# Optimization experiments

Measured on AMD Instinct MI355X. Metric: run time of the kernel, lower is better.

The kernel has to match this reference:

```python
import jax, jax.numpy as jnp
import numpy as np

N_NODES = 100000
N_EDGES = 3200000
NFEAT = 512
HIDDEN = 256
NCLASS = 64
K = 10
ALPHA = 0.1


def setup_inputs() -> dict:
    key = jax.random.key(0)
    ks = jax.random.split(key, 5)
    x = jax.random.normal(ks[0], (N_NODES, NFEAT), dtype=jnp.float32)
    edge_index = jax.random.randint(ks[1], (2, N_EDGES), 0, N_NODES, dtype=jnp.int64)
    W1 = jax.random.normal(ks[2], (NFEAT, HIDDEN), dtype=jnp.float32) * (1.0 / np.sqrt(NFEAT))
    b1 = jnp.zeros((HIDDEN,), dtype=jnp.float32)
    W2 = jax.random.normal(ks[3], (HIDDEN, NCLASS), dtype=jnp.float32) * (1.0 / np.sqrt(HIDDEN))
    b2 = jnp.zeros((NCLASS,), dtype=jnp.float32)
    # PPR initialization of GPR coefficients: alpha*(1-alpha)^k, last = (1-alpha)^K
    temp_np = ALPHA * (1.0 - ALPHA) ** np.arange(K + 1)
    temp_np[-1] = (1.0 - ALPHA) ** K
    temp = jnp.asarray(temp_np, dtype=jnp.float32)
    return {"x": x, "edge_index": edge_index, "W1": W1, "b1": b1, "W2": W2, "b2": b2, "temp": temp}


def reference(x, edge_index, W1, b1, W2, b2, temp):
    N = x.shape[0]
    # --- gcn_norm: add self-loops, symmetric normalization ---
    loop = jnp.arange(N, dtype=edge_index.dtype)
    row = jnp.concatenate([edge_index[0], loop])  # source nodes
    col = jnp.concatenate([edge_index[1], loop])  # target nodes
    ones = jnp.ones(row.shape[0], dtype=x.dtype)
    deg = jax.ops.segment_sum(ones, col, num_segments=N)
    dinv = jnp.where(deg > 0, jax.lax.rsqrt(deg), jnp.zeros((), x.dtype))
    norm = dinv[row] * dinv[col]  # [E+N]

    # --- MLP (eval mode: dropout is identity) ---
    h = jax.nn.relu(x @ W1 + b1) @ W2 + b2  # [N, nclass]

    # --- GPR propagation: hidden = sum_k temp[k] * (Ahat^k h) ---
    hidden = h * temp[0]
    for k in range(K):
        h = jax.ops.segment_sum(norm[:, None] * h[row], col, num_segments=N)
        hidden = hidden + temp[k + 1] * h

    return jax.nn.log_softmax(hidden, axis=1)
```

## Files before the change

### kernel.cpp

```cpp
#include <hip/hip_runtime.h>
#include <hip/hip_bf16.h>
#include <math.h>

#define N_NODES 100000
#define N_EDGES 3200000
#define NFEAT   512
#define HIDDEN  256
#define NCLASS  64
#define K_HOPS  10

typedef unsigned short bfbits;
typedef __attribute__((ext_vector_type(8))) short short8x;
typedef __attribute__((ext_vector_type(4))) float float4x;

__device__ __forceinline__ float bf2f(bfbits u) {
    union { unsigned int i; float f; } v; v.i = ((unsigned int)u) << 16; return v.f;
}
__device__ __forceinline__ bfbits f2bf(float f) {
    union { float f; unsigned int i; } v; v.f = f;
    unsigned int b = v.i + 0x7FFFu + ((v.i >> 16) & 1u);
    return (bfbits)(b >> 16);
}
__device__ __forceinline__ float2 unpack2(unsigned int u) {
    float2 r;
    union { unsigned int i; float f; } a, b;
    a.i = (u & 0xFFFFu) << 16; b.i = u & 0xFFFF0000u;
    r.x = a.f; r.y = b.f; return r;
}
__device__ __forceinline__ unsigned int pack2(float x, float y) {
    return ((unsigned int)f2bf(x)) | (((unsigned int)f2bf(y)) << 16);
}


__global__ void init_kernel(int* __restrict__ degi, int* __restrict__ cursor, int n) {
    int i = blockIdx.x * blockDim.x + threadIdx.x;
    if (i < n) { degi[i] = 1; cursor[i] = 0; }
}

__global__ void count_kernel(const int* __restrict__ col, int* __restrict__ degi, int e) {
    int i = blockIdx.x * blockDim.x + threadIdx.x;
    if (i < e) atomicAdd(&degi[col[i]], 1);
}

__global__ void dinv_kernel(const int* __restrict__ degi, float* __restrict__ dinv, int n) {
    int i = blockIdx.x * blockDim.x + threadIdx.x;
    if (i < n) dinv[i] = rsqrtf((float)degi[i]);
}

#define SCAN_NB 256
#define SCAN_NT 256

__global__ __launch_bounds__(SCAN_NT) void scan_phase1(const int* __restrict__ degi,
                                                       int* __restrict__ blocksums, int n) {
    int chunk = (n + SCAN_NB - 1) / SCAN_NB;
    int beg = blockIdx.x * chunk;
    int end = min(beg + chunk, n);
    int tid = threadIdx.x;
    int s = 0;
    for (int i = beg + tid; i < end; i += SCAN_NT) s += degi[i] - 1;
    __shared__ int wsum[SCAN_NT / 64];
#pragma unroll
    for (int o = 32; o > 0; o >>= 1) s += __shfl_xor(s, o, 64);
    if ((tid & 63) == 0) wsum[tid >> 6] = s;
    __syncthreads();
    if (tid == 0) {
        int t = 0;
#pragma unroll
        for (int w = 0; w < SCAN_NT / 64; ++w) t += wsum[w];
        blocksums[blockIdx.x] = t;
    }
}

__global__ __launch_bounds__(SCAN_NB) void scan_phase2(const int* __restrict__ blocksums,
                                                       int* __restrict__ blockbase) {
    __shared__ int t[SCAN_NB];
    int tid = threadIdx.x;
    t[tid] = blocksums[tid];
    __syncthreads();
    for (int d = 1; d < SCAN_NB; d <<= 1) {
        int v = (tid >= d) ? t[tid - d] : 0;
        __syncthreads();
        t[tid] += v;
        __syncthreads();
    }
    blockbase[tid] = (tid > 0) ? t[tid - 1] : 0;
}

__global__ __launch_bounds__(SCAN_NT) void scan_phase3(const int* __restrict__ degi,
                                                       const int* __restrict__ blockbase,
                                                       int* __restrict__ offs, int n) {
    __shared__ int tsum[SCAN_NT];
    int chunk = (n + SCAN_NB - 1) / SCAN_NB;
    int beg = blockIdx.x * chunk;
    int end = min(beg + chunk, n);
    int tid = threadIdx.x;
    int sub = (chunk + SCAN_NT - 1) / SCAN_NT;
    int tb = beg + tid * sub;
    int te = min(tb + sub, end);
    int s = 0;
    for (int i = tb; i < te; ++i) s += degi[i] - 1;
    tsum[tid] = s;
    __syncthreads();
    for (int d = 1; d < SCAN_NT; d <<= 1) {
        int v = (tid >= d) ? tsum[tid - d] : 0;
        __syncthreads();
        tsum[tid] += v;
        __syncthreads();
    }
    int run = blockbase[blockIdx.x] + ((tid > 0) ? tsum[tid - 1] : 0);
    for (int i = tb; i < te; ++i) { offs[i] = run; run += degi[i] - 1; }
    if (blockIdx.x == SCAN_NB - 1 && tid == SCAN_NT - 1)
        offs[n] = blockbase[blockIdx.x] + tsum[SCAN_NT - 1];
}

__global__ void scatter_kernel(const int* __restrict__ row, const int* __restrict__ col,
                               const int* __restrict__ offs, int* __restrict__ cursor,
                               int* __restrict__ srcs, int e) {
    int i = blockIdx.x * blockDim.x + threadIdx.x;
    if (i < e) {
        int c = col[i];
        int p = offs[c] + atomicAdd(&cursor[c], 1);
        srcs[p] = row[i];
    }
}

__global__ __launch_bounds__(256) void transpose_cast(const float* __restrict__ src,
                                                      bfbits* __restrict__ dst,
                                                      int K, int N) {
    __shared__ float tile[32][33];
    int kt = blockIdx.x * 32, nt = blockIdx.y * 32;
    int c = threadIdx.x & 31, r0 = threadIdx.x >> 5;
#pragma unroll
    for (int i = 0; i < 4; ++i) {
        int r = r0 + i * 8;
        tile[r][c] = src[(size_t)(kt + r) * N + nt + c];
    }
    __syncthreads();
#pragma unroll
    for (int i = 0; i < 4; ++i) {
        int r = r0 + i * 8;
        dst[(size_t)(nt + r) * K + kt + c] = f2bf(tile[c][r]);
    }
}

#define LDP 40

__global__ __launch_bounds__(512) void gemm1_mfma(const float* __restrict__ X,
                                                  const bfbits* __restrict__ W1T,
                                                  const float* __restrict__ bias,
                                                  bfbits* __restrict__ H, int M) {
    __shared__ short x_lds[128 * LDP];
    __shared__ short w_lds[256 * LDP];
    int tid = threadIdx.x;
    int wave = tid >> 6, lane = tid & 63;
    int l15 = lane & 15, quad = lane >> 4;
    int fslot = wave & 3, nslot = wave >> 2;
    int m0 = blockIdx.x * 128;

    float4x acc[4][4];
#pragma unroll
    for (int i = 0; i < 4; ++i)
#pragma unroll
        for (int j = 0; j < 4; ++j) acc[i][j] = (float4x){0.f, 0.f, 0.f, 0.f};

    for (int kb = 0; kb < NFEAT; kb += 32) {
#pragma unroll
        for (int c = 0; c < 2; ++c) {
            int qid = tid + c * 512;
            int node = qid >> 3;
            int k0 = (qid & 7) * 4;
            int row = m0 + node;
            float4 v = make_float4(0.f, 0.f, 0.f, 0.f);
            if (row < M) v = *reinterpret_cast<const float4*>(X + (size_t)row * NFEAT + kb + k0);
            ushort4 u;
            u.x = f2bf(v.x); u.y = f2bf(v.y); u.z = f2bf(v.z); u.w = f2bf(v.w);
            *reinterpret_cast<ushort4*>(&x_lds[node * LDP + k0]) = u;
        }
#pragma unroll
        for (int c = 0; c < 2; ++c) {
            int qid = tid + c * 512;
            int feat = qid >> 2;
            int k0 = (qid & 3) * 8;
            uint4 w = *reinterpret_cast<const uint4*>(W1T + (size_t)feat * NFEAT + kb + k0);
            *reinterpret_cast<uint4*>(&w_lds[feat * LDP + k0]) = w;
        }
        __syncthreads();
        short8x af[4], bf[4];
#pragma unroll
        for (int t = 0; t < 4; ++t) {
            af[t] = *reinterpret_cast<const short8x*>(&w_lds[(fslot * 64 + t * 16 + l15) * LDP + quad * 8]);
            bf[t] = *reinterpret_cast<const short8x*>(&x_lds[(nslot * 64 + t * 16 + l15) * LDP + quad * 8]);
        }
#pragma unroll
        for (int ft = 0; ft < 4; ++ft)
#pragma unroll
            for (int nt = 0; nt < 4; ++nt)
                acc[ft][nt] = __builtin_amdgcn_mfma_f32_16x16x32_bf16(af[ft], bf[nt], acc[ft][nt], 0, 0, 0);
        __syncthreads();
    }
#pragma unroll
    for (int ft = 0; ft < 4; ++ft) {
        int f = fslot * 64 + ft * 16 + quad * 4;
        float4 b = *reinterpret_cast<const float4*>(bias + f);
#pragma unroll
        for (int nt = 0; nt < 4; ++nt) {
            int node = m0 + nslot * 64 + nt * 16 + l15;
            if (node >= M) continue;
            float4x a = acc[ft][nt];
            ushort4 u;
            u.x = f2bf(fmaxf(a.x + b.x, 0.f));
            u.y = f2bf(fmaxf(a.y + b.y, 0.f));
            u.z = f2bf(fmaxf(a.z + b.z, 0.f));
            u.w = f2bf(fmaxf(a.w + b.w, 0.f));
            *reinterpret_cast<ushort4*>(H + (size_t)node * HIDDEN + f) = u;
        }
    }
}

__global__ __launch_bounds__(256) void gemm2_mfma(const bfbits* __restrict__ Hm,
                                                  const bfbits* __restrict__ W2T,
                                                  const float* __restrict__ bias,
                                                  const float* __restrict__ dinv,
                                                  bfbits* __restrict__ g0,
                                                  float* __restrict__ S,
                                                  const float* __restrict__ temp, int M) {
    __shared__ short h_lds[256 * LDP];
    __shared__ short w_lds[64 * LDP];
    int tid = threadIdx.x;
    int wave = tid >> 6, lane = tid & 63;
    int l15 = lane & 15, quad = lane >> 4;
    int nslot = wave;
    int m0 = blockIdx.x * 256;

    float4x acc[4][4];
#pragma unroll
    for (int i = 0; i < 4; ++i)
#pragma unroll
        for (int j = 0; j < 4; ++j) acc[i][j] = (float4x){0.f, 0.f, 0.f, 0.f};

    for (int kb = 0; kb < HIDDEN; kb += 32) {
#pragma unroll
        for (int c = 0; c < 4; ++c) {
            int qid = tid + c * 256;
            int node = qid >> 2;
            int k0 = (qid & 3) * 8;
            int row = m0 + node;
            uint4 v = make_uint4(0u, 0u, 0u, 0u);
            if (row < M) v = *reinterpret_cast<const uint4*>(Hm + (size_t)row * HIDDEN + kb + k0);
            *reinterpret_cast<uint4*>(&h_lds[node * LDP + k0]) = v;
        }
        {
            int feat = tid >> 2;
            int k0 = (tid & 3) * 8;
            uint4 w = *reinterpret_cast<const uint4*>(W2T + (size_t)feat * HIDDEN + kb + k0);
            *reinterpret_cast<uint4*>(&w_lds[feat * LDP + k0]) = w;
        }
        __syncthreads();
        short8x af[4], bf[4];
#pragma unroll
        for (int t = 0; t < 4; ++t) {
            af[t] = *reinterpret_cast<const short8x*>(&w_lds[(t * 16 + l15) * LDP + quad * 8]);
            bf[t] = *reinterpret_cast<const short8x*>(&h_lds[(nslot * 64 + t * 16 + l15) * LDP + quad * 8]);
        }
#pragma unroll
        for (int ft = 0; ft < 4; ++ft)
#pragma unroll
            for (int nt = 0; nt < 4; ++nt)
                acc[ft][nt] = __builtin_amdgcn_mfma_f32_16x16x32_bf16(af[ft], bf[nt], acc[ft][nt], 0, 0, 0);
        __syncthreads();
    }
    float t0 = temp[0];
#pragma unroll
    for (int nt = 0; nt < 4; ++nt) {
        int node = m0 + nslot * 64 + nt * 16 + l15;
        if (node >= M) continue;
        float di = dinv[node];
        float s0 = t0 / di;
#pragma unroll
        for (int ft = 0; ft < 4; ++ft) {
            int f = ft * 16 + quad * 4;
            float4 b = *reinterpret_cast<const float4*>(bias + f);
            float4x a = acc[ft][nt];
            float4 v = make_float4(a.x + b.x, a.y + b.y, a.z + b.z, a.w + b.w);
            ushort4 u;
            u.x = f2bf(di * v.x); u.y = f2bf(di * v.y);
            u.z = f2bf(di * v.z); u.w = f2bf(di * v.w);
            *reinterpret_cast<ushort4*>(g0 + (size_t)node * NCLASS + f) = u;
            float4 sv = make_float4(s0 * v.x, s0 * v.y, s0 * v.z, s0 * v.w);
            *reinterpret_cast<float4*>(S + (size_t)node * NCLASS + f) = sv;
        }
    }
}

__global__ __launch_bounds__(256) void propagate_kernel(const int* __restrict__ offs,
                                                        const int* __restrict__ srcs,
                                                        const float* __restrict__ dinv,
                                                        const uint2* __restrict__ gin,
                                                        uint2* __restrict__ gout,
                                                        float* __restrict__ S,
                                                        const float* __restrict__ temp,
                                                        int kidx, int n) {
    int node = (blockIdx.x * blockDim.x + threadIdx.x) >> 6;
    int lane = threadIdx.x & 63;
    if (node >= n) return;
    int q = lane >> 4, sub = lane & 15;
    float tk = temp[kidx];
    int beg = offs[node], end = offs[node + 1];

    uint2 gs = gin[(size_t)node * 16 + sub];
    float4 acc = make_float4(0.f, 0.f, 0.f, 0.f);
    if (q == 0) {
        float2 lo = unpack2(gs.x), hi = unpack2(gs.y);
        acc = make_float4(lo.x, lo.y, hi.x, hi.y);
    }

    int e = beg;
    for (; e + 16 <= end; e += 16) {
#pragma unroll
        for (int j = 0; j < 4; ++j) {
            int s = srcs[e + j * 4 + q];
            uint2 u = gin[(size_t)s * 16 + sub];
            float2 lo = unpack2(u.x), hi = unpack2(u.y);
            acc.x += lo.x; acc.y += lo.y; acc.z += hi.x; acc.w += hi.y;
        }
    }
    for (; e < end; e += 4) {
        int idx = e + q;
        int sidx = (idx < end) ? idx : e;
        int s = srcs[sidx];
        uint2 u = gin[(size_t)s * 16 + sub];
        if (idx < end) {
            float2 lo = unpack2(u.x), hi = unpack2(u.y);
            acc.x += lo.x; acc.y += lo.y; acc.z += hi.x; acc.w += hi.y;
        }
    }

    acc.x += __shfl_xor(acc.x, 16, 64); acc.y += __shfl_xor(acc.y, 16, 64);
    acc.z += __shfl_xor(acc.z, 16, 64); acc.w += __shfl_xor(acc.w, 16, 64);
    acc.x += __shfl_xor(acc.x, 32, 64); acc.y += __shfl_xor(acc.y, 32, 64);
    acc.z += __shfl_xor(acc.z, 32, 64); acc.w += __shfl_xor(acc.w, 32, 64);

    if (q == 0) {
        float di = dinv[node];
        float dd = di * di;
        gout[(size_t)node * 16 + sub] =
            make_uint2(pack2(dd * acc.x, dd * acc.y), pack2(dd * acc.z, dd * acc.w));
        float4* Sp = reinterpret_cast<float4*>(S + (size_t)node * 64 + sub * 4);
        float4 sv = *Sp;
        sv.x += tk * acc.x; sv.y += tk * acc.y;
        sv.z += tk * acc.z; sv.w += tk * acc.w;
        *Sp = sv;
    }
}

__global__ __launch_bounds__(256) void logsoftmax_kernel(const float* __restrict__ S,
                                                         const float* __restrict__ dinv,
                                                         float* __restrict__ out, int n) {
    int node = (blockIdx.x * blockDim.x + threadIdx.x) >> 6;
    int lane = threadIdx.x & 63;
    if (node >= n) return;
    float v = dinv[node] * S[(size_t)node * 64 + lane];
    float m = v;
#pragma unroll
    for (int o = 32; o > 0; o >>= 1) m = fmaxf(m, __shfl_xor(m, o, 64));
    float ex = expf(v - m);
    float s = ex;
#pragma unroll
    for (int o = 32; o > 0; o >>= 1) s += __shfl_xor(s, o, 64);
    out[(size_t)node * 64 + lane] = v - m - logf(s);
}


extern "C" void kernel_launch(void* const* d_in, const int* in_sizes, int n_in,
                              void* d_out, int out_size, void* d_ws, size_t ws_size,
                              hipStream_t stream) {
    const float* x    = (const float*)d_in[0];
    const int*   ei   = (const int*)d_in[1];
    const int*   row  = ei;
    const int*   col  = ei + N_EDGES;
    const float* W1   = (const float*)d_in[2];
    const float* b1   = (const float*)d_in[3];
    const float* W2   = (const float*)d_in[4];
    const float* b2   = (const float*)d_in[5];
    const float* temp = (const float*)d_in[6];
    float*       out  = (float*)d_out;

    char* ws = (char*)d_ws;
    size_t off = 0;
    auto alloc = [&](size_t bytes) -> void* {
        void* p = ws + off;
        off += (bytes + 255) & ~(size_t)255;
        return p;
    };
    int*    degi   = (int*)   alloc((size_t)N_NODES * 4);
    float*  dinv   = (float*) alloc((size_t)N_NODES * 4);
    int*    offs   = (int*)   alloc((size_t)(N_NODES + 1) * 4);
    int*    cursor = (int*)   alloc((size_t)N_NODES * 4);
    int*    srcs   = (int*)   alloc((size_t)N_EDGES * 4);
    int*    bsums  = (int*)   alloc((size_t)SCAN_NB * 4);
    int*    bbase  = (int*)   alloc((size_t)SCAN_NB * 4);
    bfbits* W1T    = (bfbits*)alloc((size_t)HIDDEN * NFEAT * 2);
    bfbits* W2T    = (bfbits*)alloc((size_t)NCLASS * HIDDEN * 2);
    bfbits* h_mlp  = (bfbits*)alloc((size_t)N_NODES * HIDDEN * 2);
    bfbits* g_a    = (bfbits*)alloc((size_t)N_NODES * NCLASS * 2);
    bfbits* g_b    = (bfbits*)alloc((size_t)N_NODES * NCLASS * 2);
    float*  S      = (float*) alloc((size_t)N_NODES * NCLASS * 4);

    init_kernel<<<(N_NODES + 255) / 256, 256, 0, stream>>>(degi, cursor, N_NODES);
    count_kernel<<<(N_EDGES + 255) / 256, 256, 0, stream>>>(col, degi, N_EDGES);
    dinv_kernel<<<(N_NODES + 255) / 256, 256, 0, stream>>>(degi, dinv, N_NODES);
    scan_phase1<<<SCAN_NB, SCAN_NT, 0, stream>>>(degi, bsums, N_NODES);
    scan_phase2<<<1, SCAN_NB, 0, stream>>>(bsums, bbase);
    scan_phase3<<<SCAN_NB, SCAN_NT, 0, stream>>>(degi, bbase, offs, N_NODES);
    scatter_kernel<<<(N_EDGES + 255) / 256, 256, 0, stream>>>(row, col, offs, cursor,
                                                              srcs, N_EDGES);

    dim3 gt1(NFEAT / 32, HIDDEN / 32);
    transpose_cast<<<gt1, 256, 0, stream>>>(W1, W1T, NFEAT, HIDDEN);
    dim3 gt2(HIDDEN / 32, NCLASS / 32);
    transpose_cast<<<gt2, 256, 0, stream>>>(W2, W2T, HIDDEN, NCLASS);

    gemm1_mfma<<<(N_NODES + 127) / 128, 512, 0, stream>>>(x, W1T, b1, h_mlp, N_NODES);
    gemm2_mfma<<<(N_NODES + 255) / 256, 256, 0, stream>>>(h_mlp, W2T, b2, dinv, g_a, S,
                                                          temp, N_NODES);

    int pgrid = (N_NODES * 64 + 255) / 256;
    for (int k = 0; k < K_HOPS; ++k) {
        bfbits* gi = (k & 1) ? g_b : g_a;
        bfbits* go = (k & 1) ? g_a : g_b;
        propagate_kernel<<<pgrid, 256, 0, stream>>>(offs, srcs, dinv,
                                                    (const uint2*)gi, (uint2*)go, S,
                                                    temp, k + 1, N_NODES);
    }

    logsoftmax_kernel<<<pgrid, 256, 0, stream>>>(S, dinv, out, N_NODES);
}
```

Before: 1.369 ms.

## Split propagation into feature chunks with chunk-major layout for cache locality

Stores propagated features as four chunk-major planes of 16 features each and runs propagation once per chunk per hop. This shrinks the randomly gathered working set per launch so it is more likely to stay in L2. In exchange the CSR index arrays are re-read once per chunk, launch count quadruples, and each gather moves only 32 bytes per edge.

```diff
diff --git a/kernel.cpp b/kernel.cpp
--- a/kernel.cpp
+++ b/kernel.cpp
@@ -8,6 +8,7 @@
 #define HIDDEN  256
 #define NCLASS  64
 #define K_HOPS  10
+#define NCHUNK  4
 
 typedef unsigned short bfbits;
 typedef __attribute__((ext_vector_type(8))) short short8x;
@@ -285,67 +286,71 @@
             ushort4 u;
             u.x = f2bf(di * v.x); u.y = f2bf(di * v.y);
             u.z = f2bf(di * v.z); u.w = f2bf(di * v.w);
-            *reinterpret_cast<ushort4*>(g0 + (size_t)node * NCLASS + f) = u;
+            *reinterpret_cast<ushort4*>(g0 + ((size_t)ft * M + node) * 16 + quad * 4) = u;
             float4 sv = make_float4(s0 * v.x, s0 * v.y, s0 * v.z, s0 * v.w);
-            *reinterpret_cast<float4*>(S + (size_t)node * NCLASS + f) = sv;
-        }
-    }
-}
-
-__global__ __launch_bounds__(256) void propagate_kernel(const int* __restrict__ offs,
-                                                        const int* __restrict__ srcs,
-                                                        const float* __restrict__ dinv,
-                                                        const uint2* __restrict__ gin,
-                                                        uint2* __restrict__ gout,
-                                                        float* __restrict__ S,
-                                                        const float* __restrict__ temp,
-                                                        int kidx, int n) {
+            *reinterpret_cast<float4*>(S + (size_t)node * 64 + f) = sv;
+        }
+    }
+}
+
+__global__ __launch_bounds__(256) void propagate_chunk(const int* __restrict__ offs,
+                                                       const int* __restrict__ srcs,
+                                                       const float* __restrict__ dinv,
+                                                       const uint2* __restrict__ gin_all,
+                                                       uint2* __restrict__ gout_all,
+                                                       float* __restrict__ S,
+                                                       const float* __restrict__ temp,
+                                                       int kidx, int chunk, int n) {
     int node = (blockIdx.x * blockDim.x + threadIdx.x) >> 6;
     int lane = threadIdx.x & 63;
     if (node >= n) return;
-    int q = lane >> 4, sub = lane & 15;
+    int eslot = lane >> 2, sub = lane & 3;
+    const uint2* gin = gin_all + (size_t)chunk * n * 4;
+    uint2* gout = gout_all + (size_t)chunk * n * 4;
     float tk = temp[kidx];
     int beg = offs[node], end = offs[node + 1];
 
-    uint2 gs = gin[(size_t)node * 16 + sub];
     float4 acc = make_float4(0.f, 0.f, 0.f, 0.f);
-    if (q == 0) {
+    if (eslot == 0) {
+        uint2 gs = gin[(size_t)node * 4 + sub];
         float2 lo = unpack2(gs.x), hi = unpack2(gs.y);
         acc = make_float4(lo.x, lo.y, hi.x, hi.y);
     }
 
     int e = beg;
-    for (; e + 16 <= end; e += 16) {
-#pragma unroll
-        for (int j = 0; j < 4; ++j) {
-            int s = srcs[e + j * 4 + q];
-            uint2 u = gin[(size_t)s * 16 + sub];
+    for (; e + 32 <= end; e += 32) {
+        int s0 = srcs[e + eslot];
+        int s1 = srcs[e + 16 + eslot];
+        uint2 u0 = gin[(size_t)s0 * 4 + sub];
+        uint2 u1 = gin[(size_t)s1 * 4 + sub];
+        float2 lo0 = unpack2(u0.x), hi0 = unpack2(u0.y);
+        float2 lo1 = unpack2(u1.x), hi1 = unpack2(u1.y);
+        acc.x += lo0.x + lo1.x; acc.y += lo0.y + lo1.y;
+        acc.z += hi0.x + hi1.x; acc.w += hi0.y + hi1.y;
+    }
+    for (; e < end; e += 16) {
+        int idx = e + eslot;
+        bool v = idx < end;
+        int s = srcs[v ? idx : end - 1];
+        uint2 u = gin[(size_t)s * 4 + sub];
+        if (v) {
             float2 lo = unpack2(u.x), hi = unpack2(u.y);
             acc.x += lo.x; acc.y += lo.y; acc.z += hi.x; acc.w += hi.y;
         }
     }
-    for (; e < end; e += 4) {
-        int idx = e + q;
-        int sidx = (idx < end) ? idx : e;
-        int s = srcs[sidx];
-        uint2 u = gin[(size_t)s * 16 + sub];
-        if (idx < end) {
-            float2 lo = unpack2(u.x), hi = unpack2(u.y);
-            acc.x += lo.x; acc.y += lo.y; acc.z += hi.x; acc.w += hi.y;
-        }
-    }
-
-    acc.x += __shfl_xor(acc.x, 16, 64); acc.y += __shfl_xor(acc.y, 16, 64);
-    acc.z += __shfl_xor(acc.z, 16, 64); acc.w += __shfl_xor(acc.w, 16, 64);
-    acc.x += __shfl_xor(acc.x, 32, 64); acc.y += __shfl_xor(acc.y, 32, 64);
-    acc.z += __shfl_xor(acc.z, 32, 64); acc.w += __shfl_xor(acc.w, 32, 64);
-
-    if (q == 0) {
+
+#pragma unroll
+    for (int o = 4; o < 64; o <<= 1) {
+        acc.x += __shfl_xor(acc.x, o, 64); acc.y += __shfl_xor(acc.y, o, 64);
+        acc.z += __shfl_xor(acc.z, o, 64); acc.w += __shfl_xor(acc.w, o, 64);
+    }
+
+    if (lane < 4) {
         float di = dinv[node];
         float dd = di * di;
-        gout[(size_t)node * 16 + sub] =
+        gout[(size_t)node * 4 + sub] =
             make_uint2(pack2(dd * acc.x, dd * acc.y), pack2(dd * acc.z, dd * acc.w));
-        float4* Sp = reinterpret_cast<float4*>(S + (size_t)node * 64 + sub * 4);
+        float4* Sp = reinterpret_cast<float4*>(S + (size_t)node * 64 + chunk * 16 + sub * 4);
         float4 sv = *Sp;
         sv.x += tk * acc.x; sv.y += tk * acc.y;
         sv.z += tk * acc.z; sv.w += tk * acc.w;
@@ -428,9 +433,11 @@
     for (int k = 0; k < K_HOPS; ++k) {
         bfbits* gi = (k & 1) ? g_b : g_a;
         bfbits* go = (k & 1) ? g_a : g_b;
-        propagate_kernel<<<pgrid, 256, 0, stream>>>(offs, srcs, dinv,
-                                                    (const uint2*)gi, (uint2*)go, S,
-                                                    temp, k + 1, N_NODES);
+        for (int c = 0; c < NCHUNK; ++c) {
+            propagate_chunk<<<pgrid, 256, 0, stream>>>(offs, srcs, dinv,
+                                                       (const uint2*)gi, (uint2*)go, S,
+                                                       temp, k + 1, c, N_NODES);
+        }
     }
 
     logsoftmax_kernel<<<pgrid, 256, 0, stream>>>(S, dinv, out, N_NODES);
```

Measured after the change: 2.262 ms. 1.65x slower.

## Tile propagation by source-node range to keep gathered features cache-resident

Applied to the files above, without the earlier changes.

Splits the edge lists into four buckets per destination node, keyed by which quarter of the source-node range an edge comes from. Each hop then runs four passes, one per bucket, with partial sums kept in a new fp32 buffer A. The aim is to keep the gathered bf16 feature rows for each pass (25000 nodes × 128 B) small enough to stay in cache, so random gathers hit L2 instead of HBM. In exchange it quadruples launches and offset reads and adds read-modify-write traffic on A. It also rewrites the inner gather loop to an 8-edge unrolled form using nontemporal loads.

```diff
diff --git a/kernel.cpp b/kernel.cpp
--- a/kernel.cpp
+++ b/kernel.cpp
@@ -8,10 +8,15 @@
 #define HIDDEN  256
 #define NCLASS  64
 #define K_HOPS  10
+#define NTILE   4
+#define TQ      25000
+#define NVIRT   (N_NODES * NTILE)
 
 typedef unsigned short bfbits;
 typedef __attribute__((ext_vector_type(8))) short short8x;
 typedef __attribute__((ext_vector_type(4))) float float4x;
+typedef __attribute__((ext_vector_type(4))) float f4v;
+typedef __attribute__((ext_vector_type(2))) unsigned int u2v;
 
 __device__ __forceinline__ float bf2f(bfbits u) {
     union { unsigned int i; float f; } v; v.i = ((unsigned int)u) << 16; return v.f;
@@ -32,32 +37,40 @@
 }
 
 
-__global__ void init_kernel(int* __restrict__ degi, int* __restrict__ cursor, int n) {
+__global__ void init_kernel(int* __restrict__ bcnt, int* __restrict__ cursor, int n) {
     int i = blockIdx.x * blockDim.x + threadIdx.x;
-    if (i < n) { degi[i] = 1; cursor[i] = 0; }
-}
-
-__global__ void count_kernel(const int* __restrict__ col, int* __restrict__ degi, int e) {
+    if (i < n) { bcnt[i] = 0; cursor[i] = 0; }
+}
+
+__global__ void count_kernel(const int* __restrict__ row, const int* __restrict__ col,
+                             int* __restrict__ bcnt, int e) {
     int i = blockIdx.x * blockDim.x + threadIdx.x;
-    if (i < e) atomicAdd(&degi[col[i]], 1);
-}
-
-__global__ void dinv_kernel(const int* __restrict__ degi, float* __restrict__ dinv, int n) {
+    if (i < e) {
+        int r = row[i], c = col[i];
+        atomicAdd(&bcnt[c * NTILE + r / TQ], 1);
+    }
+}
+
+__global__ void dinv_kernel(const int* __restrict__ bcnt, float* __restrict__ dinv, int n) {
     int i = blockIdx.x * blockDim.x + threadIdx.x;
-    if (i < n) dinv[i] = rsqrtf((float)degi[i]);
+    if (i < n) {
+        int d = 1 + bcnt[i * NTILE] + bcnt[i * NTILE + 1] + bcnt[i * NTILE + 2]
+                  + bcnt[i * NTILE + 3];
+        dinv[i] = rsqrtf((float)d);
+    }
 }
 
 #define SCAN_NB 256
 #define SCAN_NT 256
 
-__global__ __launch_bounds__(SCAN_NT) void scan_phase1(const int* __restrict__ degi,
+__global__ __launch_bounds__(SCAN_NT) void scan_phase1(const int* __restrict__ bcnt,
                                                        int* __restrict__ blocksums, int n) {
     int chunk = (n + SCAN_NB - 1) / SCAN_NB;
     int beg = blockIdx.x * chunk;
     int end = min(beg + chunk, n);
     int tid = threadIdx.x;
     int s = 0;
-    for (int i = beg + tid; i < end; i += SCAN_NT) s += degi[i] - 1;
+    for (int i = beg + tid; i < end; i += SCAN_NT) s += bcnt[i];
     __shared__ int wsum[SCAN_NT / 64];
 #pragma unroll
     for (int o = 32; o > 0; o >>= 1) s += __shfl_xor(s, o, 64);
@@ -86,7 +99,7 @@
     blockbase[tid] = (tid > 0) ? t[tid - 1] : 0;
 }
 
-__global__ __launch_bounds__(SCAN_NT) void scan_phase3(const int* __restrict__ degi,
+__global__ __launch_bounds__(SCAN_NT) void scan_phase3(const int* __restrict__ bcnt,
                                                        const int* __restrict__ blockbase,
                                                        int* __restrict__ offs, int n) {
     __shared__ int tsum[SCAN_NT];
@@ -98,7 +111,7 @@
     int tb = beg + tid * sub;
     int te = min(tb + sub, end);
     int s = 0;
-    for (int i = tb; i < te; ++i) s += degi[i] - 1;
+    for (int i = tb; i < te; ++i) s += bcnt[i];
     tsum[tid] = s;
     __syncthreads();
     for (int d = 1; d < SCAN_NT; d <<= 1) {
@@ -108,7 +121,7 @@
         __syncthreads();
     }
     int run = blockbase[blockIdx.x] + ((tid > 0) ? tsum[tid - 1] : 0);
-    for (int i = tb; i < te; ++i) { offs[i] = run; run += degi[i] - 1; }
+    for (int i = tb; i < te; ++i) { offs[i] = run; run += bcnt[i]; }
     if (blockIdx.x == SCAN_NB - 1 && tid == SCAN_NT - 1)
         offs[n] = blockbase[blockIdx.x] + tsum[SCAN_NT - 1];
 }
@@ -118,9 +131,10 @@
                                int* __restrict__ srcs, int e) {
     int i = blockIdx.x * blockDim.x + threadIdx.x;
     if (i < e) {
-        int c = col[i];
-        int p = offs[c] + atomicAdd(&cursor[c], 1);
-        srcs[p] = row[i];
+        int r = row[i], c = col[i];
+        int vk = c * NTILE + r / TQ;
+        int p = offs[vk] + atomicAdd(&cursor[vk], 1);
+        srcs[p] = r;
     }
 }
 
@@ -287,50 +301,46 @@
             u.z = f2bf(di * v.z); u.w = f2bf(di * v.w);
             *reinterpret_cast<ushort4*>(g0 + (size_t)node * NCLASS + f) = u;
             float4 sv = make_float4(s0 * v.x, s0 * v.y, s0 * v.z, s0 * v.w);
-            *reinterpret_cast<float4*>(S + (size_t)node * NCLASS + f) = sv;
-        }
-    }
-}
-
-__global__ __launch_bounds__(256) void propagate_kernel(const int* __restrict__ offs,
-                                                        const int* __restrict__ srcs,
-                                                        const float* __restrict__ dinv,
-                                                        const uint2* __restrict__ gin,
-                                                        uint2* __restrict__ gout,
-                                                        float* __restrict__ S,
-                                                        const float* __restrict__ temp,
-                                                        int kidx, int n) {
+            *reinterpret_cast<float4*>(S + (size_t)node * 64 + f) = sv;
+        }
+    }
+}
+
+__global__ __launch_bounds__(256) void propagate_pass(const int* __restrict__ offs2,
+                                                      const int* __restrict__ srcs,
+                                                      const float* __restrict__ dinv,
+                                                      const uint2* __restrict__ gin,
+                                                      uint2* __restrict__ gout,
+                                                      float* __restrict__ A,
+                                                      float* __restrict__ S,
+                                                      const float* __restrict__ temp,
+                                                      int kidx, int tile, int n) {
     int node = (blockIdx.x * blockDim.x + threadIdx.x) >> 6;
     int lane = threadIdx.x & 63;
     if (node >= n) return;
-    int q = lane >> 4, sub = lane & 15;
-    float tk = temp[kidx];
-    int beg = offs[node], end = offs[node + 1];
-
-    uint2 gs = gin[(size_t)node * 16 + sub];
+    int grp = lane >> 4, sub = lane & 15;
+    int beg = offs2[node * NTILE + tile], end = offs2[node * NTILE + tile + 1];
+
     float4 acc = make_float4(0.f, 0.f, 0.f, 0.f);
-    if (q == 0) {
+    if (tile == 0 && grp == 0) {
+        uint2 gs = gin[(size_t)node * 16 + sub];
         float2 lo = unpack2(gs.x), hi = unpack2(gs.y);
         acc = make_float4(lo.x, lo.y, hi.x, hi.y);
     }
 
-    int e = beg;
-    for (; e + 16 <= end; e += 16) {
-#pragma unroll
-        for (int j = 0; j < 4; ++j) {
-            int s = srcs[e + j * 4 + q];
-            uint2 u = gin[(size_t)s * 16 + sub];
-            float2 lo = unpack2(u.x), hi = unpack2(u.y);
+    for (int e = beg; e < end; e += 8) {
+        int i0 = e + grp, i1 = e + 4 + grp;
+        int c0 = min(i0, end - 1), c1 = min(i1, end - 1);
+        int s0 = __builtin_nontemporal_load(srcs + c0);
+        int s1 = __builtin_nontemporal_load(srcs + c1);
+        uint2 u0 = gin[(size_t)s0 * 16 + sub];
+        uint2 u1 = gin[(size_t)s1 * 16 + sub];
+        if (i0 < end) {
+            float2 lo = unpack2(u0.x), hi = unpack2(u0.y);
             acc.x += lo.x; acc.y += lo.y; acc.z += hi.x; acc.w += hi.y;
         }
-    }
-    for (; e < end; e += 4) {
-        int idx = e + q;
-        int sidx = (idx < end) ? idx : e;
-        int s = srcs[sidx];
-        uint2 u = gin[(size_t)s * 16 + sub];
-        if (idx < end) {
-            float2 lo = unpack2(u.x), hi = unpack2(u.y);
+        if (i1 < end) {
+            float2 lo = unpack2(u1.x), hi = unpack2(u1.y);
             acc.x += lo.x; acc.y += lo.y; acc.z += hi.x; acc.w += hi.y;
         }
     }
@@ -340,16 +350,30 @@
     acc.x += __shfl_xor(acc.x, 32, 64); acc.y += __shfl_xor(acc.y, 32, 64);
     acc.z += __shfl_xor(acc.z, 32, 64); acc.w += __shfl_xor(acc.w, 32, 64);
 
-    if (q == 0) {
-        float di = dinv[node];
-        float dd = di * di;
-        gout[(size_t)node * 16 + sub] =
-            make_uint2(pack2(dd * acc.x, dd * acc.y), pack2(dd * acc.z, dd * acc.w));
-        float4* Sp = reinterpret_cast<float4*>(S + (size_t)node * 64 + sub * 4);
-        float4 sv = *Sp;
-        sv.x += tk * acc.x; sv.y += tk * acc.y;
-        sv.z += tk * acc.z; sv.w += tk * acc.w;
-        *Sp = sv;
+    if (grp == 0) {
+        f4v* Ap = (f4v*)(A + (size_t)node * 64 + sub * 4);
+        if (tile == 0) {
+            f4v av; av.x = acc.x; av.y = acc.y; av.z = acc.z; av.w = acc.w;
+            __builtin_nontemporal_store(av, Ap);
+        } else if (tile < NTILE - 1) {
+            f4v a0 = __builtin_nontemporal_load(Ap);
+            a0.x += acc.x; a0.y += acc.y; a0.z += acc.z; a0.w += acc.w;
+            __builtin_nontemporal_store(a0, Ap);
+        } else {
+            f4v a0 = __builtin_nontemporal_load(Ap);
+            float tx = a0.x + acc.x, ty = a0.y + acc.y;
+            float tz = a0.z + acc.z, tw = a0.w + acc.w;
+            float di = dinv[node];
+            float dd = di * di;
+            float tk = temp[kidx];
+            gout[(size_t)node * 16 + sub] =
+                make_uint2(pack2(dd * tx, dd * ty), pack2(dd * tz, dd * tw));
+            float4* Sp = reinterpret_cast<float4*>(S + (size_t)node * 64 + sub * 4);
+            float4 sv = *Sp;
+            sv.x += tk * tx; sv.y += tk * ty;
+            sv.z += tk * tz; sv.w += tk * tw;
+            *Sp = sv;
+        }
     }
 }
 
@@ -392,10 +416,10 @@
         off += (bytes + 255) & ~(size_t)255;
         return p;
     };
-    int*    degi   = (int*)   alloc((size_t)N_NODES * 4);
+    int*    bcnt   = (int*)   alloc((size_t)NVIRT * 4);
+    int*    offs2  = (int*)   alloc((size_t)(NVIRT + 1) * 4);
+    int*    cursor = (int*)   alloc((size_t)NVIRT * 4);
     float*  dinv   = (float*) alloc((size_t)N_NODES * 4);
-    int*    offs   = (int*)   alloc((size_t)(N_NODES + 1) * 4);
-    int*    cursor = (int*)   alloc((size_t)N_NODES * 4);
     int*    srcs   = (int*)   alloc((size_t)N_EDGES * 4);
     int*    bsums  = (int*)   alloc((size_t)SCAN_NB * 4);
     int*    bbase  = (int*)   alloc((size_t)SCAN_NB * 4);
@@ -405,14 +429,15 @@
     bfbits* g_a    = (bfbits*)alloc((size_t)N_NODES * NCLASS * 2);
     bfbits* g_b    = (bfbits*)alloc((size_t)N_NODES * NCLASS * 2);
     float*  S      = (float*) alloc((size_t)N_NODES * NCLASS * 4);
-
-    init_kernel<<<(N_NODES + 255) / 256, 256, 0, stream>>>(degi, cursor, N_NODES);
-    count_kernel<<<(N_EDGES + 255) / 256, 256, 0, stream>>>(col, degi, N_EDGES);
-    dinv_kernel<<<(N_NODES + 255) / 256, 256, 0, stream>>>(degi, dinv, N_NODES);
-    scan_phase1<<<SCAN_NB, SCAN_NT, 0, stream>>>(degi, bsums, N_NODES);
+    float*  A      = (float*) alloc((size_t)N_NODES * NCLASS * 4);
+
+    init_kernel<<<(NVIRT + 255) / 256, 256, 0, stream>>>(bcnt, cursor, NVIRT);
+    count_kernel<<<(N_EDGES + 255) / 256, 256, 0, stream>>>(row, col, bcnt, N_EDGES);
+    dinv_kernel<<<(N_NODES + 255) / 256, 256, 0, stream>>>(bcnt, dinv, N_NODES);
+    scan_phase1<<<SCAN_NB, SCAN_NT, 0, stream>>>(bcnt, bsums, NVIRT);
     scan_phase2<<<1, SCAN_NB, 0, stream>>>(bsums, bbase);
-    scan_phase3<<<SCAN_NB, SCAN_NT, 0, stream>>>(degi, bbase, offs, N_NODES);
-    scatter_kernel<<<(N_EDGES + 255) / 256, 256, 0, stream>>>(row, col, offs, cursor,
+    scan_phase3<<<SCAN_NB, SCAN_NT, 0, stream>>>(bcnt, bbase, offs2, NVIRT);
+    scatter_kernel<<<(N_EDGES + 255) / 256, 256, 0, stream>>>(row, col, offs2, cursor,
                                                               srcs, N_EDGES);
 
     dim3 gt1(NFEAT / 32, HIDDEN / 32);
@@ -428,9 +453,11 @@
     for (int k = 0; k < K_HOPS; ++k) {
         bfbits* gi = (k & 1) ? g_b : g_a;
         bfbits* go = (k & 1) ? g_a : g_b;
-        propagate_kernel<<<pgrid, 256, 0, stream>>>(offs, srcs, dinv,
-                                                    (const uint2*)gi, (uint2*)go, S,
-                                                    temp, k + 1, N_NODES);
+        for (int t = 0; t < NTILE; ++t) {
+            propagate_pass<<<pgrid, 256, 0, stream>>>(offs2, srcs, dinv,
+                                                      (const uint2*)gi, (uint2*)go,
+                                                      A, S, temp, k + 1, t, N_NODES);
+        }
     }
 
     logsoftmax_kernel<<<pgrid, 256, 0, stream>>>(S, dinv, out, N_NODES);
```

After: 2.737 ms. 100.0% more time.
